# Optimization experiments

Hardware: AMD Instinct MI355X
Metric: run time of the kernel (lower is better)

The kernel has to match this reference:

```python
import jax, jax.numpy as jnp
import numpy as np

L, D, H, T, DFF = 4, 1024, 8, 1000, 4096
HS = D // H  # 128


def _rope_cos_sin():
    # theta_i = 10000^(-2(i-1)/dim) for i in 1..dim/2 (dim = head size)
    i = jnp.arange(1, HS // 2 + 1, dtype=jnp.float32)
    theta = jnp.power(jnp.float32(10000.0), -2.0 * (i - 1.0) / HS)
    t = jnp.arange(T, dtype=jnp.float32)
    ang = t[:, None] * theta[None, :]              # (T, HS/2)
    return jnp.cos(ang), jnp.sin(ang)


def _apply_rope(x, cos, sin):
    # x: (B,H,T,HS); interpret last dim as HS/2 complex pairs and multiply by e^{i t theta}
    xs = x.reshape(*x.shape[:-1], HS // 2, 2)
    xr, xi = xs[..., 0], xs[..., 1]
    c = cos[None, None, :, :]
    s = sin[None, None, :, :]
    out_r = xr * c - xi * s
    out_i = xr * s + xi * c
    return jnp.stack([out_r, out_i], axis=-1).reshape(x.shape)


def _ln(x, g, b, eps=1e-5):
    m = jnp.mean(x, axis=-1, keepdims=True)
    v = jnp.mean((x - m) ** 2, axis=-1, keepdims=True)
    return (x - m) * jax.lax.rsqrt(v + eps) * g + b


def setup_inputs() -> dict:
    key = jax.random.key(0)
    ks = jax.random.split(key, 16)
    sc = 0.02
    inp = {
        'x':   jax.random.normal(ks[0], (8, T, D), jnp.float32),
        'Wq':  sc * jax.random.normal(ks[1], (L, D, D), jnp.float32),
        'Wk':  sc * jax.random.normal(ks[2], (L, D, D), jnp.float32),
        'Wv':  sc * jax.random.normal(ks[3], (L, D, D), jnp.float32),
        'Wpk': sc * jax.random.normal(ks[4], (L, T, T), jnp.float32),
        'bpk': jnp.zeros((L, T), jnp.float32),
        'Wpv': sc * jax.random.normal(ks[5], (L, T, T), jnp.float32),
        'bpv': jnp.zeros((L, T), jnp.float32),
        'ln1_g': jnp.ones((L, D), jnp.float32),
        'ln1_b': jnp.zeros((L, D), jnp.float32),
        'W1':  sc * jax.random.normal(ks[6], (L, DFF, D), jnp.float32),
        'b1':  jnp.zeros((L, DFF), jnp.float32),
        'W2':  sc * jax.random.normal(ks[7], (L, D, DFF), jnp.float32),
        'b2':  jnp.zeros((L, D), jnp.float32),
        'ln2_g': jnp.ones((L, D), jnp.float32),
        'ln2_b': jnp.zeros((L, D), jnp.float32),
    }
    return inp


def reference(x, Wq, Wk, Wv, Wpk, bpk, Wpv, bpv, ln1_g, ln1_b,
              W1, b1, W2, b2, ln2_g, ln2_b):
    B = x.shape[0]
    cos, sin = _rope_cos_sin()
    out = x
    for l in range(L):
        src = out
        # QKV projections (bias=False), split into heads: (B,H,T,HS)
        q = jnp.einsum('btc,dc->btd', src, Wq[l]).reshape(B, T, H, HS).transpose(0, 2, 1, 3)
        k = jnp.einsum('btc,dc->btd', src, Wk[l]).reshape(B, T, H, HS).transpose(0, 2, 1, 3)
        v = jnp.einsum('btc,dc->btd', src, Wv[l]).reshape(B, T, H, HS).transpose(0, 2, 1, 3)
        # ChunkedLinear over the SEQUENCE axis for K and V (single 1000x1000 block)
        k = jnp.einsum('bhtd,ut->bhud', k, Wpk[l]) + bpk[l][None, None, :, None]
        v = jnp.einsum('bhtd,ut->bhud', v, Wpv[l]) + bpv[l][None, None, :, None]
        # RoPE on q and k
        q = _apply_rope(q, cos, sin)
        k = _apply_rope(k, cos, sin)
        # Full (non-causal; mask is commented out in source) softmax attention
        scores = jnp.einsum('bhqd,bhkd->bhqk', q, k) / jnp.sqrt(jnp.float32(HS))
        attn = jax.nn.softmax(scores, axis=-1)
        y = jnp.einsum('bhqk,bhkd->bhqd', attn, v)
        y = y.transpose(0, 2, 1, 3).reshape(B, T, D)  # NOTE: no output proj (faithful to source)
        src = _ln(src + y, ln1_g[l], ln1_b[l])
        h = jax.nn.gelu(jnp.einsum('btd,fd->btf', src, W1[l]) + b1[l], approximate=False)
        src = _ln(src + jnp.einsum('btf,df->btd', h, W2[l]) + b2[l], ln2_g[l], ln2_b[l])
        out = src
    return out
```

## Files before the change

### kernel.cpp

```cpp
#include <hip/hip_runtime.h>
#include <cstdint>
#include <cstddef>


typedef unsigned short u16;
typedef unsigned int u32;
typedef __attribute__((ext_vector_type(8))) short s16x8;
typedef __attribute__((ext_vector_type(4))) float f32x4;

#define DEV static __device__ __forceinline__

DEV float bf2f(u16 u) { union { u32 u; float f; } v; v.u = ((u32)u) << 16; return v.f; }
DEV u16 f2bf(float f) {
  union { float f; u32 u; } v; v.f = f;
  return (u16)((v.u + 0x7fffu + ((v.u >> 16) & 1u)) >> 16);
}

#define MFMA(acc_, a_, b_) \
  asm volatile("v_mfma_f32_16x16x32_bf16 %0, %1, %2, %0" : "+v"(acc_) : "v"(a_), "v"(b_))

#define GLD16(g_, l_) \
  __builtin_amdgcn_global_load_lds((const __attribute__((address_space(1))) void*)(g_), \
                                   (__attribute__((address_space(3))) void*)(l_), 16, 0, 0)

static constexpr int T_ = 1000, D_ = 1024, H_ = 8, HS_ = 128, B_ = 8;
static constexpr int BT_ = B_ * T_;

__global__ void tab_kernel(float* __restrict__ ct, float* __restrict__ st) {
  const int id = blockIdx.x * 256 + threadIdx.x;
  const int i = id & 63, t = id >> 6;
  const float theta = powf(10000.f, -(float)i * (1.f / 64.f));
  const float ang = (float)t * theta;
  ct[id] = cosf(ang);
  st[id] = sinf(ang);
}

__global__ void convert_kernel(const float* __restrict__ in, u16* __restrict__ out, int n) {
  const int i = (blockIdx.x * 256 + threadIdx.x) * 4;
  if (i < n) {
    const float4 v = *(const float4*)(in + i);
    uint2 pk;
    pk.x = (u32)f2bf(v.x) | ((u32)f2bf(v.y) << 16);
    pk.y = (u32)f2bf(v.z) | ((u32)f2bf(v.w) << 16);
    *(uint2*)(out + i) = pk;
  }
}

__global__ __launch_bounds__(256) void transpose_kernel(const u16* __restrict__ in,
                                                        u16* __restrict__ out, int cb) {
  __shared__ u16 tile[64][72];
  const int tt = blockIdx.x, dt = blockIdx.y, b = blockIdx.z;
  const int tid = threadIdx.x;
  const int r = tid >> 2, cq = (tid & 3) << 4;
  const int t = tt * 64 + r;
#pragma unroll
  for (int v = 0; v < 2; ++v) {
    s16x8 val = {};
    if (t < T_) val = *(const s16x8*)(in + (size_t)(b * 1000 + t) * 3072 + cb + dt * 64 + cq + v * 8);
    *(s16x8*)&tile[r][cq + v * 8] = val;
  }
  __syncthreads();
  const int d = dt * 64 + r;
  u16 vals[16];
#pragma unroll
  for (int j = 0; j < 16; ++j) vals[j] = tile[cq + j][r];
  u16* o = out + (size_t)b * 1048576 + (size_t)d * 1024 + tt * 64 + cq;
  *(s16x8*)o = *(s16x8*)&vals[0];
  *(s16x8*)(o + 8) = *(s16x8*)&vals[8];
}

template <int BIAS, bool ACT, bool OUTBF>
__global__ __launch_bounds__(256) void gemm_nt(
    const u16* __restrict__ A, const u16* __restrict__ B, void* __restrict__ Cv,
    const float* __restrict__ bias, int M, int N, int K, int lda, int ldb, int ldc,
    long sA, long sB, long sC) {
  __shared__ alignas(16) u16 As[128 * 32];
  __shared__ alignas(16) u16 Bs[128 * 32];
  const int z = blockIdx.z;
  A += (size_t)z * (size_t)sA;
  B += (size_t)z * (size_t)sB;
  const int m0 = blockIdx.y * 128, n0 = blockIdx.x * 128;
  const int tid = threadIdx.x;
  const int wid = tid >> 6, lane = tid & 63;
  const int wr = wid >> 1, wc = wid & 1;
  const int l15 = lane & 15, l4 = lane >> 4;
  const int srow = tid >> 2, scol = (tid & 3) << 3;
  const int mA0 = min(m0 + srow, M - 1);
  const int mA1 = min(m0 + 64 + srow, M - 1);
  const int nB0 = min(n0 + srow, N - 1);
  const int nB1 = min(n0 + 64 + srow, N - 1);
  const u16* gA0 = A + (size_t)mA0 * lda + scol;
  const u16* gA1 = A + (size_t)mA1 * lda + scol;
  const u16* gB0 = B + (size_t)nB0 * ldb + scol;
  const u16* gB1 = B + (size_t)nB1 * ldb + scol;
  u16* lA0 = As + tid * 8;  u16* lA1 = As + (256 + tid) * 8;
  u16* lB0 = Bs + tid * 8;  u16* lB1 = Bs + (256 + tid) * 8;
  f32x4 acc[4][4] = {};
  const int KT = K >> 5;
  for (int kt = 0; kt < KT; ++kt) {
    const int kb = kt << 5;
    GLD16(gA0 + kb, lA0);
    GLD16(gA1 + kb, lA1);
    GLD16(gB0 + kb, lB0);
    GLD16(gB1 + kb, lB1);
    __syncthreads();
    s16x8 af[4], bfr[4];
#pragma unroll
    for (int i = 0; i < 4; ++i)
      af[i] = *(const s16x8*)&As[(wr * 64 + i * 16 + l15) * 32 + l4 * 8];
#pragma unroll
    for (int i = 0; i < 4; ++i)
      bfr[i] = *(const s16x8*)&Bs[(wc * 64 + i * 16 + l15) * 32 + l4 * 8];
#pragma unroll
    for (int mi = 0; mi < 4; ++mi)
#pragma unroll
      for (int ni = 0; ni < 4; ++ni) MFMA(acc[mi][ni], af[mi], bfr[ni]);
    __syncthreads();
  }
  asm volatile("s_nop 7\n\ts_nop 7"
               : "+v"(acc[3][0]), "+v"(acc[3][1]), "+v"(acc[3][2]), "+v"(acc[3][3]));
#pragma unroll
  for (int mi = 0; mi < 4; ++mi) {
#pragma unroll
    for (int ni = 0; ni < 4; ++ni) {
      const int colg = n0 + wc * 64 + ni * 16 + l15;
#pragma unroll
      for (int r = 0; r < 4; ++r) {
        const int rowg = m0 + wr * 64 + mi * 16 + l4 * 4 + r;
        if (rowg < M && colg < N) {
          float v = acc[mi][ni][r];
          if (BIAS == 1) v += bias[rowg];
          if (BIAS == 2) v += bias[colg];
          if (ACT) v = 0.5f * v * (1.0f + erff(v * 0.70710678118654752f));
          const size_t idx = (size_t)z * (size_t)sC + (size_t)rowg * ldc + colg;
          if (OUTBF) ((u16*)Cv)[idx] = f2bf(v);
          else       ((float*)Cv)[idx] = v;
        }
      }
    }
  }
}

__global__ __launch_bounds__(256) void rope_kernel(u16* __restrict__ X, int ld,
                                                   const float* __restrict__ ct,
                                                   const float* __restrict__ st) {
  const int id = blockIdx.x * 256 + threadIdx.x;
  const int i = id & 63;
  const int h = (id >> 6) & 7;
  const int bt = id >> 9;
  const int t = bt % 1000;
  const size_t base = (size_t)bt * ld + h * HS_ + i * 2;
  u32* p = (u32*)(X + base);
  const u32 w = *p;
  const float xr = bf2f((u16)(w & 0xffffu));
  const float xi = bf2f((u16)(w >> 16));
  const float c = ct[t * 64 + i], s = st[t * 64 + i];
  const float outr = xr * c - xi * s;
  const float outi = xr * s + xi * c;
  *p = (u32)f2bf(outr) | ((u32)f2bf(outi) << 16);
}

__global__ __launch_bounds__(256) void attn_kernel(const u16* __restrict__ Q, int ldq,
                                                   const u16* __restrict__ Km,
                                                   const u16* __restrict__ Vmt,
                                                   float* __restrict__ Y) {
  __shared__ alignas(16) u16 Ks[64][136];
  __shared__ alignas(16) u16 Vts[128][72];
  __shared__ alignas(16) u16 Ps[4][32][72];
  const int qt = blockIdx.x;
  const int bh = blockIdx.y;
  const int b = bh >> 3, h = bh & 7;
  const int tid = threadIdx.x;
  const int w = tid >> 6, lane = tid & 63;
  const int l15 = lane & 15, l4 = lane >> 4;
  const size_t qbase = (size_t)b * 1000 * ldq + h * HS_;
  const size_t kbase = (size_t)b * 1024000 + h * HS_;
  const size_t vbase = (size_t)b * 1048576 + (size_t)(h * HS_) * 1024;
  const int q0 = qt * 128 + w * 32;
  s16x8 aq[2][4];
#pragma unroll
  for (int qf = 0; qf < 2; ++qf) {
    const int qrow = q0 + qf * 16 + l15;
#pragma unroll
    for (int c = 0; c < 4; ++c) {
      s16x8 v = {};
      if (qrow < T_) v = *(const s16x8*)(Q + qbase + (size_t)qrow * ldq + c * 32 + l4 * 8);
      aq[qf][c] = v;
    }
  }
  f32x4 acc[2][8] = {};
  float m_run[2][4], l_run[2][4];
#pragma unroll
  for (int qf = 0; qf < 2; ++qf)
#pragma unroll
    for (int r = 0; r < 4; ++r) { m_run[qf][r] = -1e30f; l_run[qf][r] = 0.f; }
  const float SCALE = 0.08838834764831845f;
  for (int kt = 0; kt < 16; ++kt) {
    {
      const int r = tid >> 2, c0 = (tid & 3) << 5;
      const int kk = kt * 64 + r;
#pragma unroll
      for (int v = 0; v < 4; ++v) {
        s16x8 val = {};
        if (kk < T_) val = *(const s16x8*)(Km + kbase + (size_t)kk * 1024 + c0 + v * 8);
        *(s16x8*)&Ks[r][c0 + v * 8] = val;
      }
      const int r2 = tid >> 1, c2s = (tid & 1) << 5;
#pragma unroll
      for (int v = 0; v < 4; ++v) {
        const s16x8 val = *(const s16x8*)(Vmt + vbase + (size_t)r2 * 1024 + kt * 64 + c2s + v * 8);
        *(s16x8*)&Vts[r2][c2s + v * 8] = val;
      }
    }
    __syncthreads();
    f32x4 sacc[2][4] = {};
#pragma unroll
    for (int c = 0; c < 4; ++c) {
      s16x8 bk[4];
#pragma unroll
      for (int f = 0; f < 4; ++f) bk[f] = *(const s16x8*)&Ks[f * 16 + l15][c * 32 + l4 * 8];
#pragma unroll
      for (int qf = 0; qf < 2; ++qf)
#pragma unroll
        for (int f = 0; f < 4; ++f) MFMA(sacc[qf][f], aq[qf][c], bk[f]);
    }
    asm volatile("s_nop 7\n\ts_nop 7"
                 : "+v"(sacc[0][0]), "+v"(sacc[0][1]), "+v"(sacc[0][2]), "+v"(sacc[0][3]),
                   "+v"(sacc[1][0]), "+v"(sacc[1][1]), "+v"(sacc[1][2]), "+v"(sacc[1][3]));
#pragma unroll
    for (int qf = 0; qf < 2; ++qf) {
      float sv[4][4];
#pragma unroll
      for (int f = 0; f < 4; ++f) {
        const int key = kt * 64 + f * 16 + l15;
#pragma unroll
        for (int r = 0; r < 4; ++r) sv[f][r] = (key < T_) ? sacc[qf][f][r] * SCALE : -1e30f;
      }
#pragma unroll
      for (int r = 0; r < 4; ++r) {
        float mx = fmaxf(fmaxf(sv[0][r], sv[1][r]), fmaxf(sv[2][r], sv[3][r]));
#pragma unroll
        for (int off = 8; off >= 1; off >>= 1) mx = fmaxf(mx, __shfl_xor(mx, off));
        const float mn = fmaxf(m_run[qf][r], mx);
        const float corr = __expf(m_run[qf][r] - mn);
        m_run[qf][r] = mn;
        float rs = 0.f;
#pragma unroll
        for (int f = 0; f < 4; ++f) {
          const float p = __expf(sv[f][r] - mn);
          rs += p;
          Ps[w][qf * 16 + l4 * 4 + r][f * 16 + l15] = f2bf(p);
        }
#pragma unroll
        for (int off = 8; off >= 1; off >>= 1) rs += __shfl_xor(rs, off);
        l_run[qf][r] = l_run[qf][r] * corr + rs;
#pragma unroll
        for (int n = 0; n < 8; ++n) acc[qf][n][r] *= corr;
      }
    }
    asm volatile("s_waitcnt lgkmcnt(0)" ::: "memory");
#pragma unroll
    for (int c2 = 0; c2 < 2; ++c2) {
      s16x8 pa[2];
#pragma unroll
      for (int qf = 0; qf < 2; ++qf)
        pa[qf] = *(const s16x8*)&Ps[w][qf * 16 + l15][c2 * 32 + l4 * 8];
#pragma unroll
      for (int n = 0; n < 8; ++n) {
        const s16x8 vb = *(const s16x8*)&Vts[n * 16 + l15][c2 * 32 + l4 * 8];
#pragma unroll
        for (int qf = 0; qf < 2; ++qf) MFMA(acc[qf][n], pa[qf], vb);
      }
    }
    __syncthreads();
  }
  asm volatile("s_nop 7\n\ts_nop 7"
               : "+v"(acc[0][6]), "+v"(acc[0][7]), "+v"(acc[1][6]), "+v"(acc[1][7]));
#pragma unroll
  for (int qf = 0; qf < 2; ++qf)
#pragma unroll
    for (int n = 0; n < 8; ++n)
#pragma unroll
      for (int r = 0; r < 4; ++r) {
        const int q = q0 + qf * 16 + l4 * 4 + r;
        if (q < T_)
          Y[(size_t)(b * 1000 + q) * 1024 + h * HS_ + n * 16 + l15] = acc[qf][n][r] / l_run[qf][r];
      }
}

__global__ __launch_bounds__(256) void addln_kernel(float* __restrict__ src,
                                                    const float* __restrict__ add,
                                                    const float* __restrict__ g,
                                                    const float* __restrict__ bb,
                                                    u16* __restrict__ outb) {
  const int row = blockIdx.x;
  const int tid = threadIdx.x;
  float* s = src + (size_t)row * D_;
  const float* a = add + (size_t)row * D_;
  float x[4];
  float sum = 0.f, sq = 0.f;
#pragma unroll
  for (int i = 0; i < 4; ++i) {
    const int d = tid + i * 256;
    const float v = s[d] + a[d];
    x[i] = v; sum += v; sq += v * v;
  }
#pragma unroll
  for (int off = 32; off >= 1; off >>= 1) { sum += __shfl_xor(sum, off); sq += __shfl_xor(sq, off); }
  __shared__ float red[8];
  const int wid = tid >> 6;
  if ((tid & 63) == 0) { red[wid] = sum; red[4 + wid] = sq; }
  __syncthreads();
  sum = red[0] + red[1] + red[2] + red[3];
  sq = red[4] + red[5] + red[6] + red[7];
  const float mean = sum * (1.f / 1024.f);
  const float var = sq * (1.f / 1024.f) - mean * mean;
  const float rstd = rsqrtf(var + 1e-5f);
#pragma unroll
  for (int i = 0; i < 4; ++i) {
    const int d = tid + i * 256;
    const float y = (x[i] - mean) * rstd * g[d] + bb[d];
    s[d] = y;
    outb[(size_t)row * D_ + d] = f2bf(y);
  }
}

static inline int cdiv(int a, int b) { return (a + b - 1) / b; }

extern "C" void kernel_launch(void* const* d_in, const int* in_sizes, int n_in,
                              void* d_out, int out_size, void* d_ws, size_t ws_size,
                              hipStream_t stream) {
  const float* x    = (const float*)d_in[0];
  const float* Wq   = (const float*)d_in[1];
  const float* Wk   = (const float*)d_in[2];
  const float* Wv   = (const float*)d_in[3];
  const float* Wpk  = (const float*)d_in[4];
  const float* bpk  = (const float*)d_in[5];
  const float* Wpv  = (const float*)d_in[6];
  const float* bpv  = (const float*)d_in[7];
  const float* g1   = (const float*)d_in[8];
  const float* b1ln = (const float*)d_in[9];
  const float* W1   = (const float*)d_in[10];
  const float* b1   = (const float*)d_in[11];
  const float* W2   = (const float*)d_in[12];
  const float* b2   = (const float*)d_in[13];
  const float* g2   = (const float*)d_in[14];
  const float* b2ln = (const float*)d_in[15];

  char* wsb = (char*)d_ws;
  float* cosT = (float*)(wsb + 0);
  float* sinT = (float*)(wsb + 262144);
  float* srcf = (float*)(wsb + 524288);
  u16* srcb   = (u16*)(wsb + 33292288);
  u16* QKVb   = (u16*)(wsb + 49676288);
  u16* Ttmp   = (u16*)(wsb + 98828288);
  u16* Km     = (u16*)(wsb + 115605504);
  u16* Vmt    = (u16*)(wsb + 131989504);
  u16* wbuf   = (u16*)(wsb + 148766720);
  u16* hB     = QKVb;

  u16* wqB  = wbuf + 0;
  u16* wpkB = wbuf + 3145728;
  u16* wpvB = wbuf + 4145728;
  u16* w1B  = wbuf + 5145728;
  u16* w2B  = wbuf + 9340032;

  float* yF = (float*)d_out;

  tab_kernel<<<250, 256, 0, stream>>>(cosT, sinT);
  hipMemcpyAsync(srcf, x, (size_t)BT_ * D_ * sizeof(float), hipMemcpyDeviceToDevice, stream);
  convert_kernel<<<cdiv(BT_ * D_, 1024), 256, 0, stream>>>(x, srcb, BT_ * D_);

  for (int l = 0; l < 4; ++l) {
    convert_kernel<<<cdiv(1048576, 1024), 256, 0, stream>>>(Wq + (size_t)l * 1048576, wqB, 1048576);
    convert_kernel<<<cdiv(1048576, 1024), 256, 0, stream>>>(Wk + (size_t)l * 1048576, wqB + 1048576, 1048576);
    convert_kernel<<<cdiv(1048576, 1024), 256, 0, stream>>>(Wv + (size_t)l * 1048576, wqB + 2097152, 1048576);
    convert_kernel<<<cdiv(1000000, 1024), 256, 0, stream>>>(Wpk + (size_t)l * 1000000, wpkB, 1000000);
    convert_kernel<<<cdiv(1000000, 1024), 256, 0, stream>>>(Wpv + (size_t)l * 1000000, wpvB, 1000000);
    convert_kernel<<<cdiv(4194304, 1024), 256, 0, stream>>>(W1 + (size_t)l * 4194304, w1B, 4194304);
    convert_kernel<<<cdiv(4194304, 1024), 256, 0, stream>>>(W2 + (size_t)l * 4194304, w2B, 4194304);

    gemm_nt<0, false, true><<<dim3(24, 63, 1), 256, 0, stream>>>(
        srcb, wqB, QKVb, nullptr, BT_, 3072, 1024, 1024, 1024, 3072, 0, 0, 0);

    transpose_kernel<<<dim3(16, 16, 8), 256, 0, stream>>>(QKVb, Ttmp, 1024);
    gemm_nt<1, false, true><<<dim3(8, 8, 8), 256, 0, stream>>>(
        wpkB, Ttmp, Km, bpk + (size_t)l * 1000, 1000, 1024, 1024,
        1000, 1024, 1024, 0L, 1048576L, 1024000L);

    transpose_kernel<<<dim3(16, 16, 8), 256, 0, stream>>>(QKVb, Ttmp, 2048);
    gemm_nt<2, false, true><<<dim3(8, 8, 8), 256, 0, stream>>>(
        Ttmp, wpvB, Vmt, bpv + (size_t)l * 1000, 1024, 1000, 1024,
        1024, 1000, 1024, 1048576L, 0L, 1048576L);

    rope_kernel<<<16000, 256, 0, stream>>>(QKVb, 3072, cosT, sinT);
    rope_kernel<<<16000, 256, 0, stream>>>(Km, 1024, cosT, sinT);

    attn_kernel<<<dim3(8, 64), 256, 0, stream>>>(QKVb, 3072, Km, Vmt, yF);

    addln_kernel<<<BT_, 256, 0, stream>>>(srcf, yF, g1 + (size_t)l * 1024,
                                          b1ln + (size_t)l * 1024, srcb);

    gemm_nt<2, true, true><<<dim3(32, 63, 1), 256, 0, stream>>>(
        srcb, w1B, hB, b1 + (size_t)l * 4096, BT_, 4096, 1024, 1024, 1024, 4096, 0, 0, 0);
    gemm_nt<2, false, false><<<dim3(8, 63, 1), 256, 0, stream>>>(
        hB, w2B, d_out, b2 + (size_t)l * 1024, BT_, 1024, 4096, 4096, 4096, 1024, 0, 0, 0);

    addln_kernel<<<BT_, 256, 0, stream>>>(srcf, yF, g2 + (size_t)l * 1024,
                                          b2ln + (size_t)l * 1024, srcb);
  }

  hipMemcpyAsync(d_out, srcf, (size_t)BT_ * D_ * sizeof(float), hipMemcpyDeviceToDevice, stream);
}
```

Before: 2.284 ms.

## Add 512-thread large-tile GEMM with triple-buffered LDS pipeline for QKV and FFN

Adds a new GEMM kernel with 256-wide (and 128 or 256-tall) output tiles, 8 waves per block, XOR-swizzled LDS layout and a three-stage global_load_lds pipeline using explicit vmcnt waits and barriers. The QKV projection and both FFN GEMMs switch to it from the older 128x128 double-buffered kernel. The goal is more operand reuse per byte loaded and better overlap of loads with MFMA work. In exchange it uses more LDS and registers per block, which lowers occupancy, and the grids are smaller, which may load the CUs unevenly on the 8000-row problem.

```diff
diff --git a/kernel.cpp b/kernel.cpp
--- a/kernel.cpp
+++ b/kernel.cpp
@@ -22,6 +22,9 @@
 #define GLD16(g_, l_) \
   __builtin_amdgcn_global_load_lds((const __attribute__((address_space(1))) void*)(g_), \
                                    (__attribute__((address_space(3))) void*)(l_), 16, 0, 0)
+
+#define BARRIER() asm volatile("s_barrier" ::: "memory")
+#define VMW(n)    asm volatile("s_waitcnt vmcnt(" #n ")" ::: "memory")
 
 static constexpr int T_ = 1000, D_ = 1024, H_ = 8, HS_ = 128, B_ = 8;
 static constexpr int BT_ = B_ * T_;
@@ -67,6 +70,111 @@
   u16* o = out + (size_t)b * 1048576 + (size_t)d * 1024 + tt * 64 + cq;
   *(s16x8*)o = *(s16x8*)&vals[0];
   *(s16x8*)(o + 8) = *(s16x8*)&vals[8];
+}
+
+template <int BMT, int BIAS, bool ACT, bool OUTBF>
+__global__ __launch_bounds__(512) void gemm_nt8(
+    const u16* __restrict__ A, const u16* __restrict__ B, void* __restrict__ Cv,
+    const float* __restrict__ bias, int M, int N, int K, int lda, int ldb, int ldc) {
+  constexpr int BM = BMT * 128;
+  constexpr int MI = 4 * BMT;
+  __shared__ alignas(16) u16 As[3][BM * 32];
+  __shared__ alignas(16) u16 Bs[3][256 * 32];
+  const int m0 = blockIdx.y * BM, n0 = blockIdx.x * 256;
+  const int tid = threadIdx.x;
+  const int wid = tid >> 6, lane = tid & 63;
+  const int wr = wid >> 2, wc = wid & 3;
+  const int l15 = lane & 15, l4 = lane >> 4;
+
+  const u16* pA[BMT];
+  const u16* pB[2];
+#pragma unroll
+  for (int j = 0; j < BMT; ++j) {
+    const int r = j * 128 + (tid >> 2);
+    const int g = (tid & 3) ^ ((r >> 1) & 3);
+    pA[j] = A + (size_t)min(m0 + r, M - 1) * lda + g * 8;
+  }
+#pragma unroll
+  for (int j = 0; j < 2; ++j) {
+    const int r = j * 128 + (tid >> 2);
+    const int g = (tid & 3) ^ ((r >> 1) & 3);
+    pB[j] = B + (size_t)(n0 + r) * ldb + g * 8;
+  }
+  int aoff[MI], boff[4];
+#pragma unroll
+  for (int mi = 0; mi < MI; ++mi) {
+    const int row = wr * (BM / 2) + mi * 16 + l15;
+    aoff[mi] = row * 32 + ((l4 ^ ((row >> 1) & 3)) * 8);
+  }
+#pragma unroll
+  for (int ni = 0; ni < 4; ++ni) {
+    const int row = wc * 64 + ni * 16 + l15;
+    boff[ni] = row * 32 + ((l4 ^ ((row >> 1) & 3)) * 8);
+  }
+
+  f32x4 acc[MI][4] = {};
+  const int KT = K >> 5;
+  int bi = 0, sb = 2;
+
+  auto STAGE = [&](int s) {
+#pragma unroll
+    for (int j = 0; j < BMT; ++j) { GLD16(pA[j], &As[s][j * 4096 + tid * 8]); pA[j] += 32; }
+#pragma unroll
+    for (int j = 0; j < 2; ++j) { GLD16(pB[j], &Bs[s][j * 4096 + tid * 8]); pB[j] += 32; }
+  };
+  auto COMPUTE = [&]() {
+    const u16* Ap = &As[bi][0];
+    const u16* Bp = &Bs[bi][0];
+    s16x8 af[MI], bfr[4];
+#pragma unroll
+    for (int mi = 0; mi < MI; ++mi) af[mi] = *(const s16x8*)(Ap + aoff[mi]);
+#pragma unroll
+    for (int ni = 0; ni < 4; ++ni) bfr[ni] = *(const s16x8*)(Bp + boff[ni]);
+    __builtin_amdgcn_s_setprio(1);
+#pragma unroll
+    for (int mi = 0; mi < MI; ++mi)
+#pragma unroll
+      for (int ni = 0; ni < 4; ++ni) MFMA(acc[mi][ni], af[mi], bfr[ni]);
+    __builtin_amdgcn_s_setprio(0);
+    bi = (bi == 2) ? 0 : bi + 1;
+  };
+
+  STAGE(0);
+  STAGE(1);
+#pragma unroll 1
+  for (int kt = 0; kt < KT - 2; ++kt) {
+    STAGE(sb); sb = (sb == 2) ? 0 : sb + 1;
+    if constexpr (BMT == 2) { VMW(8); } else { VMW(6); }
+    BARRIER();
+    COMPUTE();
+    BARRIER();
+  }
+  if constexpr (BMT == 2) { VMW(4); } else { VMW(3); }
+  BARRIER(); COMPUTE(); BARRIER();
+  VMW(0); BARRIER(); COMPUTE();
+
+  asm volatile("s_nop 7\n\ts_nop 7"
+               : "+v"(acc[MI - 1][0]), "+v"(acc[MI - 1][1]),
+                 "+v"(acc[MI - 1][2]), "+v"(acc[MI - 1][3]));
+#pragma unroll
+  for (int mi = 0; mi < MI; ++mi) {
+#pragma unroll
+    for (int ni = 0; ni < 4; ++ni) {
+      const int colg = n0 + wc * 64 + ni * 16 + l15;
+#pragma unroll
+      for (int r = 0; r < 4; ++r) {
+        const int rowg = m0 + wr * (BM / 2) + mi * 16 + l4 * 4 + r;
+        if (rowg < M) {
+          float v = acc[mi][ni][r];
+          if (BIAS == 2) v += bias[colg];
+          if (ACT) v = 0.5f * v * (1.0f + erff(v * 0.70710678118654752f));
+          const size_t idx = (size_t)rowg * ldc + colg;
+          if (OUTBF) ((u16*)Cv)[idx] = f2bf(v);
+          else       ((float*)Cv)[idx] = v;
+        }
+      }
+    }
+  }
 }
 
 template <int BIAS, bool ACT, bool OUTBF>
@@ -380,8 +488,8 @@
     convert_kernel<<<cdiv(4194304, 1024), 256, 0, stream>>>(W1 + (size_t)l * 4194304, w1B, 4194304);
     convert_kernel<<<cdiv(4194304, 1024), 256, 0, stream>>>(W2 + (size_t)l * 4194304, w2B, 4194304);
 
-    gemm_nt<0, false, true><<<dim3(24, 63, 1), 256, 0, stream>>>(
-        srcb, wqB, QKVb, nullptr, BT_, 3072, 1024, 1024, 1024, 3072, 0, 0, 0);
+    gemm_nt8<2, 0, false, true><<<dim3(12, 32), 512, 0, stream>>>(
+        srcb, wqB, QKVb, nullptr, BT_, 3072, 1024, 1024, 1024, 3072);
 
     transpose_kernel<<<dim3(16, 16, 8), 256, 0, stream>>>(QKVb, Ttmp, 1024);
     gemm_nt<1, false, true><<<dim3(8, 8, 8), 256, 0, stream>>>(
@@ -401,10 +509,10 @@
     addln_kernel<<<BT_, 256, 0, stream>>>(srcf, yF, g1 + (size_t)l * 1024,
                                           b1ln + (size_t)l * 1024, srcb);
 
-    gemm_nt<2, true, true><<<dim3(32, 63, 1), 256, 0, stream>>>(
-        srcb, w1B, hB, b1 + (size_t)l * 4096, BT_, 4096, 1024, 1024, 1024, 4096, 0, 0, 0);
-    gemm_nt<2, false, false><<<dim3(8, 63, 1), 256, 0, stream>>>(
-        hB, w2B, d_out, b2 + (size_t)l * 1024, BT_, 1024, 4096, 4096, 4096, 1024, 0, 0, 0);
+    gemm_nt8<2, 2, true, true><<<dim3(16, 32), 512, 0, stream>>>(
+        srcb, w1B, hB, b1 + (size_t)l * 4096, BT_, 4096, 1024, 1024, 1024, 4096);
+    gemm_nt8<1, 2, false, false><<<dim3(4, 63), 512, 0, stream>>>(
+        hB, w2B, d_out, b2 + (size_t)l * 1024, BT_, 1024, 4096, 4096, 4096, 1024);
 
     addln_kernel<<<BT_, 256, 0, stream>>>(srcf, yF, g2 + (size_t)l * 1024,
                                           b2ln + (size_t)l * 1024, srcb);
```

Result: slower. 2.743 ms (+20.1%).

## Add 256x256 eight-wave pipelined GEMM for QKV and FFN1 projections

Applied to the files above, without the earlier changes.

Introduces a new GEMM kernel with 256x256 output tiles, 512 threads (8 waves), double-buffered LDS filled by direct global-to-LDS loads, an XOR swizzle against bank conflicts, and split A/B prefetch interleaved with MFMA phases under raised wave priority. It replaces the 128x128 kernel for the QKV projection and the first FFN GEMM, raising arithmetic intensity per tile and overlapping loads with compute. The larger tiles mean fewer blocks (384 and 512), which may leave some compute units with uneven load, and register pressure is high with a 32-entry accumulator array.

```diff
diff --git a/kernel.cpp b/kernel.cpp
--- a/kernel.cpp
+++ b/kernel.cpp
@@ -22,6 +22,9 @@
 #define GLD16(g_, l_) \
   __builtin_amdgcn_global_load_lds((const __attribute__((address_space(1))) void*)(g_), \
                                    (__attribute__((address_space(3))) void*)(l_), 16, 0, 0)
+
+#define BARRIER() asm volatile("s_barrier" ::: "memory")
+#define VMW(n)    asm volatile("s_waitcnt vmcnt(" #n ")" ::: "memory")
 
 static constexpr int T_ = 1000, D_ = 1024, H_ = 8, HS_ = 128, B_ = 8;
 static constexpr int BT_ = B_ * T_;
@@ -67,6 +70,109 @@
   u16* o = out + (size_t)b * 1048576 + (size_t)d * 1024 + tt * 64 + cq;
   *(s16x8*)o = *(s16x8*)&vals[0];
   *(s16x8*)(o + 8) = *(s16x8*)&vals[8];
+}
+
+template <int BIAS, bool ACT, bool OUTBF>
+__global__ __launch_bounds__(512) void gemm8p(
+    const u16* __restrict__ A, const u16* __restrict__ B, void* __restrict__ Cv,
+    const float* __restrict__ bias, int M, int N, int K, int lda, int ldb, int ldc) {
+  __shared__ alignas(16) u16 lds[2][16384];
+  const int m0 = blockIdx.y * 256, n0 = blockIdx.x * 256;
+  const int tid = threadIdx.x;
+  const int lane = tid & 63, wid = tid >> 6;
+  const int wr = wid >> 2, wc = wid & 3;
+  const int l15 = lane & 15, l4 = lane >> 4;
+
+  const int srow = tid >> 2;
+  const int sg = ((tid & 3) ^ ((tid >> 3) & 3)) * 8;
+  const u16* gA0 = A + (size_t)min(m0 + srow, M - 1) * lda + sg;
+  const u16* gA1 = A + (size_t)min(m0 + 128 + srow, M - 1) * lda + sg;
+  const u16* gB0 = B + (size_t)min(n0 + srow, N - 1) * ldb + sg;
+  const u16* gB1 = B + (size_t)min(n0 + 128 + srow, N - 1) * ldb + sg;
+
+  const int gg = (l4 ^ ((l15 >> 1) & 3)) * 8;
+  const int aBase = (wr * 128 + l15) * 32 + gg;
+  const int bBase = 8192 + (wc * 64 + l15) * 32 + gg;
+
+  f32x4 acc[8][4] = {};
+  const int KT = K >> 5;
+  const int kLast = K - 32;
+
+  GLD16(gA0, &lds[0][0] + tid * 8);
+  GLD16(gA1, &lds[0][4096] + tid * 8);
+  GLD16(gB0, &lds[0][8192] + tid * 8);
+  GLD16(gB1, &lds[0][12288] + tid * 8);
+  {
+    const int kb = min(32, kLast);
+    GLD16(gB0 + kb, &lds[1][8192] + tid * 8);
+    GLD16(gB1 + kb, &lds[1][12288] + tid * 8);
+  }
+  VMW(2);
+  BARRIER();
+
+  int c = 0;
+#pragma unroll 1
+  for (int m = 0; m < KT; ++m) {
+    const u16* Lc = &lds[c][0];
+    s16x8 af[4], bf4[4];
+#pragma unroll
+    for (int mi = 0; mi < 4; ++mi) af[mi] = *(const s16x8*)(Lc + aBase + mi * 512);
+#pragma unroll
+    for (int ni = 0; ni < 4; ++ni) bf4[ni] = *(const s16x8*)(Lc + bBase + ni * 512);
+    {
+      const int kb = min((m + 1) << 5, kLast);
+      GLD16(gA0 + kb, &lds[c ^ 1][0] + tid * 8);
+      GLD16(gA1 + kb, &lds[c ^ 1][4096] + tid * 8);
+    }
+    BARRIER();
+    __builtin_amdgcn_s_setprio(1);
+#pragma unroll
+    for (int mi = 0; mi < 4; ++mi)
+#pragma unroll
+      for (int ni = 0; ni < 4; ++ni) MFMA(acc[mi][ni], af[mi], bf4[ni]);
+    __builtin_amdgcn_s_setprio(0);
+    BARRIER();
+    s16x8 ag[4];
+#pragma unroll
+    for (int mi = 0; mi < 4; ++mi) ag[mi] = *(const s16x8*)(Lc + aBase + 2048 + mi * 512);
+    {
+      const int kb = min((m + 2) << 5, kLast);
+      GLD16(gB0 + kb, &lds[c][8192] + tid * 8);
+      GLD16(gB1 + kb, &lds[c][12288] + tid * 8);
+    }
+    VMW(2);
+    BARRIER();
+    __builtin_amdgcn_s_setprio(1);
+#pragma unroll
+    for (int mi = 0; mi < 4; ++mi)
+#pragma unroll
+      for (int ni = 0; ni < 4; ++ni) MFMA(acc[4 + mi][ni], ag[mi], bf4[ni]);
+    __builtin_amdgcn_s_setprio(0);
+    BARRIER();
+    c ^= 1;
+  }
+
+  asm volatile("s_nop 7\n\ts_nop 7"
+               : "+v"(acc[7][0]), "+v"(acc[7][1]), "+v"(acc[7][2]), "+v"(acc[7][3]));
+#pragma unroll
+  for (int mi = 0; mi < 8; ++mi) {
+#pragma unroll
+    for (int ni = 0; ni < 4; ++ni) {
+      const int colg = n0 + wc * 64 + ni * 16 + l15;
+#pragma unroll
+      for (int r = 0; r < 4; ++r) {
+        const int rowg = m0 + wr * 128 + mi * 16 + l4 * 4 + r;
+        if (rowg < M) {
+          float v = acc[mi][ni][r];
+          if (BIAS == 2) v += bias[colg];
+          if (ACT) v = 0.5f * v * (1.0f + erff(v * 0.70710678118654752f));
+          const size_t idx = (size_t)rowg * ldc + colg;
+          if (OUTBF) ((u16*)Cv)[idx] = f2bf(v);
+          else       ((float*)Cv)[idx] = v;
+        }
+      }
+    }
+  }
 }
 
 template <int BIAS, bool ACT, bool OUTBF>
@@ -380,8 +486,8 @@
     convert_kernel<<<cdiv(4194304, 1024), 256, 0, stream>>>(W1 + (size_t)l * 4194304, w1B, 4194304);
     convert_kernel<<<cdiv(4194304, 1024), 256, 0, stream>>>(W2 + (size_t)l * 4194304, w2B, 4194304);
 
-    gemm_nt<0, false, true><<<dim3(24, 63, 1), 256, 0, stream>>>(
-        srcb, wqB, QKVb, nullptr, BT_, 3072, 1024, 1024, 1024, 3072, 0, 0, 0);
+    gemm8p<0, false, true><<<dim3(12, 32), 512, 0, stream>>>(
+        srcb, wqB, QKVb, nullptr, BT_, 3072, 1024, 1024, 1024, 3072);
 
     transpose_kernel<<<dim3(16, 16, 8), 256, 0, stream>>>(QKVb, Ttmp, 1024);
     gemm_nt<1, false, true><<<dim3(8, 8, 8), 256, 0, stream>>>(
@@ -401,9 +507,9 @@
     addln_kernel<<<BT_, 256, 0, stream>>>(srcf, yF, g1 + (size_t)l * 1024,
                                           b1ln + (size_t)l * 1024, srcb);
 
-    gemm_nt<2, true, true><<<dim3(32, 63, 1), 256, 0, stream>>>(
-        srcb, w1B, hB, b1 + (size_t)l * 4096, BT_, 4096, 1024, 1024, 1024, 4096, 0, 0, 0);
-    gemm_nt<2, false, false><<<dim3(8, 63, 1), 256, 0, stream>>>(
+    gemm8p<2, true, true><<<dim3(16, 32), 512, 0, stream>>>(
+        srcb, w1B, hB, b1 + (size_t)l * 4096, BT_, 4096, 1024, 1024, 1024, 4096);
+    gemm_nt<2, false, false><<<dim3(8, 63), 256, 0, stream>>>(
         hB, w2B, d_out, b2 + (size_t)l * 1024, BT_, 1024, 4096, 4096, 4096, 1024, 0, 0, 0);
 
     addln_kernel<<<BT_, 256, 0, stream>>>(srcf, yF, g2 + (size_t)l * 1024,
```

Result: slower. 2.584 ms (+13.1%).

## Double-buffer GEMM LDS tiles with prefetch and XOR-swizzled layout

Applied to the files above, without the earlier changes.

Rewrites the bf16 MFMA GEMM to use two LDS buffers, prefetching the next K tile while MFMAs run on the current one, so each iteration needs one barrier instead of two. Adds an XOR swizzle on the LDS column groups to reduce bank conflicts on fragment reads, and raises wave priority around the MFMA block. LDS use doubles. Correctness relies on the async LDS loads being waited on before the end-of-iteration barrier.

```diff
diff --git a/kernel.cpp b/kernel.cpp
--- a/kernel.cpp
+++ b/kernel.cpp
@@ -70,12 +70,12 @@
 }
 
 template <int BIAS, bool ACT, bool OUTBF>
-__global__ __launch_bounds__(256) void gemm_nt(
+__global__ __launch_bounds__(256) void gemm2p(
     const u16* __restrict__ A, const u16* __restrict__ B, void* __restrict__ Cv,
     const float* __restrict__ bias, int M, int N, int K, int lda, int ldb, int ldc,
     long sA, long sB, long sC) {
-  __shared__ alignas(16) u16 As[128 * 32];
-  __shared__ alignas(16) u16 Bs[128 * 32];
+  __shared__ alignas(16) u16 As[2][4096];
+  __shared__ alignas(16) u16 Bs[2][4096];
   const int z = blockIdx.z;
   A += (size_t)z * (size_t)sA;
   B += (size_t)z * (size_t)sB;
@@ -84,38 +84,46 @@
   const int wid = tid >> 6, lane = tid & 63;
   const int wr = wid >> 1, wc = wid & 1;
   const int l15 = lane & 15, l4 = lane >> 4;
-  const int srow = tid >> 2, scol = (tid & 3) << 3;
-  const int mA0 = min(m0 + srow, M - 1);
-  const int mA1 = min(m0 + 64 + srow, M - 1);
-  const int nB0 = min(n0 + srow, N - 1);
-  const int nB1 = min(n0 + 64 + srow, N - 1);
-  const u16* gA0 = A + (size_t)mA0 * lda + scol;
-  const u16* gA1 = A + (size_t)mA1 * lda + scol;
-  const u16* gB0 = B + (size_t)nB0 * ldb + scol;
-  const u16* gB1 = B + (size_t)nB1 * ldb + scol;
-  u16* lA0 = As + tid * 8;  u16* lA1 = As + (256 + tid) * 8;
-  u16* lB0 = Bs + tid * 8;  u16* lB1 = Bs + (256 + tid) * 8;
+  const int srow = tid >> 2;
+  const int sg = ((tid & 3) ^ ((tid >> 3) & 3)) << 3;
+  const u16* gA0 = A + (size_t)min(m0 + srow, M - 1) * lda + sg;
+  const u16* gA1 = A + (size_t)min(m0 + 64 + srow, M - 1) * lda + sg;
+  const u16* gB0 = B + (size_t)min(n0 + srow, N - 1) * ldb + sg;
+  const u16* gB1 = B + (size_t)min(n0 + 64 + srow, N - 1) * ldb + sg;
+  const int gg = (l4 ^ ((l15 >> 1) & 3)) << 3;
+  const int aBase = (wr * 64 + l15) * 32 + gg;
+  const int bBase = (wc * 64 + l15) * 32 + gg;
+
   f32x4 acc[4][4] = {};
   const int KT = K >> 5;
+  GLD16(gA0, &As[0][tid * 8]);
+  GLD16(gA1, &As[0][(256 + tid) * 8]);
+  GLD16(gB0, &Bs[0][tid * 8]);
+  GLD16(gB1, &Bs[0][(256 + tid) * 8]);
+  __syncthreads();
+  int cur = 0;
+#pragma unroll 1
   for (int kt = 0; kt < KT; ++kt) {
-    const int kb = kt << 5;
-    GLD16(gA0 + kb, lA0);
-    GLD16(gA1 + kb, lA1);
-    GLD16(gB0 + kb, lB0);
-    GLD16(gB1 + kb, lB1);
+    if (kt + 1 < KT) {
+      const int kb = (kt + 1) << 5;
+      GLD16(gA0 + kb, &As[cur ^ 1][tid * 8]);
+      GLD16(gA1 + kb, &As[cur ^ 1][(256 + tid) * 8]);
+      GLD16(gB0 + kb, &Bs[cur ^ 1][tid * 8]);
+      GLD16(gB1 + kb, &Bs[cur ^ 1][(256 + tid) * 8]);
+    }
+    s16x8 af[4], bfr[4];
+#pragma unroll
+    for (int i = 0; i < 4; ++i) af[i] = *(const s16x8*)&As[cur][aBase + i * 512];
+#pragma unroll
+    for (int i = 0; i < 4; ++i) bfr[i] = *(const s16x8*)&Bs[cur][bBase + i * 512];
+    __builtin_amdgcn_s_setprio(1);
+#pragma unroll
+    for (int mi = 0; mi < 4; ++mi)
+#pragma unroll
+      for (int ni = 0; ni < 4; ++ni) MFMA(acc[mi][ni], af[mi], bfr[ni]);
+    __builtin_amdgcn_s_setprio(0);
     __syncthreads();
-    s16x8 af[4], bfr[4];
-#pragma unroll
-    for (int i = 0; i < 4; ++i)
-      af[i] = *(const s16x8*)&As[(wr * 64 + i * 16 + l15) * 32 + l4 * 8];
-#pragma unroll
-    for (int i = 0; i < 4; ++i)
-      bfr[i] = *(const s16x8*)&Bs[(wc * 64 + i * 16 + l15) * 32 + l4 * 8];
-#pragma unroll
-    for (int mi = 0; mi < 4; ++mi)
-#pragma unroll
-      for (int ni = 0; ni < 4; ++ni) MFMA(acc[mi][ni], af[mi], bfr[ni]);
-    __syncthreads();
+    cur ^= 1;
   }
   asm volatile("s_nop 7\n\ts_nop 7"
                : "+v"(acc[3][0]), "+v"(acc[3][1]), "+v"(acc[3][2]), "+v"(acc[3][3]));
@@ -380,16 +388,16 @@
     convert_kernel<<<cdiv(4194304, 1024), 256, 0, stream>>>(W1 + (size_t)l * 4194304, w1B, 4194304);
     convert_kernel<<<cdiv(4194304, 1024), 256, 0, stream>>>(W2 + (size_t)l * 4194304, w2B, 4194304);
 
-    gemm_nt<0, false, true><<<dim3(24, 63, 1), 256, 0, stream>>>(
+    gemm2p<0, false, true><<<dim3(24, 63, 1), 256, 0, stream>>>(
         srcb, wqB, QKVb, nullptr, BT_, 3072, 1024, 1024, 1024, 3072, 0, 0, 0);
 
     transpose_kernel<<<dim3(16, 16, 8), 256, 0, stream>>>(QKVb, Ttmp, 1024);
-    gemm_nt<1, false, true><<<dim3(8, 8, 8), 256, 0, stream>>>(
+    gemm2p<1, false, true><<<dim3(8, 8, 8), 256, 0, stream>>>(
         wpkB, Ttmp, Km, bpk + (size_t)l * 1000, 1000, 1024, 1024,
         1000, 1024, 1024, 0L, 1048576L, 1024000L);
 
     transpose_kernel<<<dim3(16, 16, 8), 256, 0, stream>>>(QKVb, Ttmp, 2048);
-    gemm_nt<2, false, true><<<dim3(8, 8, 8), 256, 0, stream>>>(
+    gemm2p<2, false, true><<<dim3(8, 8, 8), 256, 0, stream>>>(
         Ttmp, wpvB, Vmt, bpv + (size_t)l * 1000, 1024, 1000, 1024,
         1024, 1000, 1024, 1048576L, 0L, 1048576L);
 
@@ -401,9 +409,9 @@
     addln_kernel<<<BT_, 256, 0, stream>>>(srcf, yF, g1 + (size_t)l * 1024,
                                           b1ln + (size_t)l * 1024, srcb);
 
-    gemm_nt<2, true, true><<<dim3(32, 63, 1), 256, 0, stream>>>(
+    gemm2p<2, true, true><<<dim3(32, 63, 1), 256, 0, stream>>>(
         srcb, w1B, hB, b1 + (size_t)l * 4096, BT_, 4096, 1024, 1024, 1024, 4096, 0, 0, 0);
-    gemm_nt<2, false, false><<<dim3(8, 63, 1), 256, 0, stream>>>(
+    gemm2p<2, false, false><<<dim3(8, 63, 1), 256, 0, stream>>>(
         hB, w2B, d_out, b2 + (size_t)l * 1024, BT_, 1024, 4096, 4096, 4096, 1024, 0, 0, 0);
 
     addln_kernel<<<BT_, 256, 0, stream>>>(srcf, yF, g2 + (size_t)l * 1024,
```

Result: no change. 2.286 ms (+0.1%).
